# Optimization experiments

Hardware: AMD Instinct MI355X
Metric: run time of the kernel (lower is better)

The kernel has to match this reference:

```python
import jax, jax.numpy as jnp
import numpy as np

N = 50000      # nodes
E = 400000     # edges (before self-loops)
F_IN = 256     # input_dim
HID = 64       # hidden_dim (per-head)
H = 4          # heads
OUT = 16       # output_dim
NEG_SLOPE = 0.2


def _gat_layer(x, W, a_src, a_dst, b, src, dst):
    # x: [N, Fin], W: [Fin, H*HID], a_src/a_dst: [H, HID], b: [H*HID]
    n = x.shape[0]
    h = (x @ W).reshape(n, H, HID)                        # [N,H,D]
    es = jnp.einsum('nhd,hd->nh', h, a_src)               # [N,H]
    ed = jnp.einsum('nhd,hd->nh', h, a_dst)               # [N,H]
    e = jax.nn.leaky_relu(es[src] + ed[dst], NEG_SLOPE)   # [E,H]
    m = jax.ops.segment_max(e, dst, num_segments=n)       # [N,H] segment softmax (stable)
    m = jnp.where(jnp.isfinite(m), m, 0.0)
    p = jnp.exp(e - m[dst])
    s = jax.ops.segment_sum(p, dst, num_segments=n)
    alpha = p / (s[dst] + 1e-16)                          # [E,H]
    out = jax.ops.segment_sum(h[src] * alpha[:, :, None], dst, num_segments=n)  # [N,H,D]
    return out.reshape(n, H * HID) + b


def setup_inputs() -> dict:
    key = jax.random.key(0)
    ks = jax.random.split(key, 24)
    lin = lambda k, i, o: (jax.random.normal(k, (i, o), jnp.float32) / np.sqrt(i)).astype(jnp.float32)
    att = lambda k: (jax.random.normal(k, (H, HID), jnp.float32) * 0.1).astype(jnp.float32)
    FH = H * HID  # 256
    inp = {
        'x': jax.random.normal(ks[0], (N, F_IN), jnp.float32),
        'edge_index': jax.random.randint(ks[1], (2, E), 0, N, dtype=jnp.int64),
        'W1': lin(ks[2], F_IN, FH), 'a1_src': att(ks[3]), 'a1_dst': att(ks[4]), 'b1': jnp.zeros((FH,), jnp.float32),
        'W2': lin(ks[5], FH, FH),   'a2_src': att(ks[6]), 'a2_dst': att(ks[7]), 'b2': jnp.zeros((FH,), jnp.float32),
        'W3': lin(ks[8], FH, FH),   'a3_src': att(ks[9]), 'a3_dst': att(ks[10]), 'b3': jnp.zeros((FH,), jnp.float32),
        'pW1': lin(ks[11], FH, HID), 'pb1': jnp.zeros((HID,), jnp.float32),
        'pW2': lin(ks[12], HID, HID), 'pb2': jnp.zeros((HID,), jnp.float32),
        'cW1': lin(ks[13], FH, HID), 'cb1': jnp.zeros((HID,), jnp.float32),
        'cW2': lin(ks[14], HID, OUT), 'cb2': jnp.zeros((OUT,), jnp.float32),
    }
    return inp


def reference(x, edge_index, W1, a1_src, a1_dst, b1, W2, a2_src, a2_dst, b2,
              W3, a3_src, a3_dst, b3, pW1, pb1, pW2, pb2, cW1, cb1, cW2, cb2):
    n = x.shape[0]
    loop = jnp.arange(n, dtype=edge_index.dtype)          # PyG GATConv adds self-loops
    src = jnp.concatenate([edge_index[0], loop])
    dst = jnp.concatenate([edge_index[1], loop])
    h = jax.nn.elu(_gat_layer(x, W1, a1_src, a1_dst, b1, src, dst))
    h = jax.nn.elu(_gat_layer(h, W2, a2_src, a2_dst, b2, src, dst))
    h = _gat_layer(h, W3, a3_src, a3_dst, b3, src, dst)   # [N, 256]
    logits = jax.nn.relu(h @ cW1 + cb1) @ cW2 + cb2       # classifier (dropout inactive, eval)
    proj = jax.nn.relu(h @ pW1 + pb1) @ pW2 + pb2         # projection head
    return jax.nn.log_softmax(logits, axis=1), proj
```

## Files before the change

kernel.cpp:

```cpp
#include <hip/hip_runtime.h>
#include <hip/hip_bf16.h>

#define NN 50000
#define EE 400000
#define TE (EE + NN)
#define SCAN_B ((NN + 255) / 256)

typedef float f4 __attribute__((ext_vector_type(4)));
typedef __bf16 b8 __attribute__((ext_vector_type(8)));
typedef unsigned short us8 __attribute__((ext_vector_type(8)));

__device__ __forceinline__ float b2f(unsigned short u) {
    union { unsigned int i; float f; } c; c.i = ((unsigned int)u) << 16; return c.f;
}
__device__ __forceinline__ unsigned short f2b(float x) {
    union { unsigned int i; float f; } c; c.f = x;
    unsigned int i = c.i;
    return (unsigned short)((i + 0x7FFFu + ((i >> 16) & 1u)) >> 16);
}
__device__ __forceinline__ int clampi(int v, int lo, int hi) {
    return v < lo ? lo : (v > hi ? hi : v);
}

#define PO_WT    0
#define PO_ATT   196608
#define PO_BT    198912
#define PO_BIAS  231680
#define PO_PW2   231808
#define PO_PB2   235904
#define PO_CW2   235968
#define PO_CB2   236992
#define PO_BT2   237008
#define PO_BIAS2 253392
#define PO_TOTAL 253520

__global__ void detect_kernel(const int* __restrict__ ei, const unsigned int* __restrict__ xw,
                              int* __restrict__ flag) {
    int lane = threadIdx.x;
    int bad = (lane < 16 && ei[2 * lane + 1] != 0) ? 1 : 0;
    int cnt = 0;
#pragma unroll
    for (int k = 0; k < 4; k++) {
        int i = lane + k * 64;
        unsigned short lo = (unsigned short)(xw[i] & 0xFFFFu);
        int e = (lo >> 7) & 0xFF;
        if (e >= 120 && e <= 132) cnt++;
    }
    unsigned long long anybad = __ballot(bad != 0);
#pragma unroll
    for (int off = 1; off < 64; off <<= 1) cnt += __shfl_xor(cnt, off, 64);
    if (lane == 0) {
        flag[0] = (anybad == 0ULL) ? 1 : 0;
        flag[1] = (cnt >= 128) ? 1 : 0;
    }
}

__global__ __launch_bounds__(256) void convx_kernel(const void* __restrict__ src,
                                                    unsigned short* __restrict__ dst,
                                                    const int* __restrict__ flag) {
    int i = blockIdx.x * 256 + threadIdx.x;
    if (i >= NN * 256 / 4) return;
    if (flag[1]) {
        ((ushort4*)dst)[i] = ((const ushort4*)src)[i];
    } else {
        float4 v = ((const float4*)src)[i];
        ushort4 o; o.x = f2b(v.x); o.y = f2b(v.y); o.z = f2b(v.z); o.w = f2b(v.w);
        ((ushort4*)dst)[i] = o;
    }
}

__device__ __forceinline__ float ldf(const void* p, int i, int bf) {
    return bf ? b2f(((const unsigned short*)p)[i]) : ((const float*)p)[i];
}
__global__ __launch_bounds__(256) void prep_kernel(
    const void* W1, const void* W2, const void* W3,
    const void* as1, const void* ad1, const void* b1,
    const void* as2, const void* ad2, const void* b2,
    const void* as3, const void* ad3, const void* b3,
    const void* pW1, const void* pb1, const void* pW2, const void* pb2,
    const void* cW1, const void* cb1, const void* cW2, const void* cb2,
    unsigned short* __restrict__ P, const int* __restrict__ flag) {
    int idx = blockIdx.x * 256 + threadIdx.x;
    if (idx >= PO_TOTAL) return;
    int bf = flag[1];
    float v;
    if (idx < PO_ATT) {
        int l = idx / 65536, r = idx % 65536;
        int n = r >> 8, k = r & 255;
        const void* W = (l == 0) ? W1 : (l == 1) ? W2 : W3;
        v = ldf(W, k * 256 + n, bf);
    } else if (idx < PO_BT) {
        int r = idx - PO_ATT;
        int l = r / 768, w = r % 768, which = w >> 8, j = w & 255;
        const void* s;
        if (which == 0) s = (l == 0) ? as1 : (l == 1) ? as2 : as3;
        else if (which == 1) s = (l == 0) ? ad1 : (l == 1) ? ad2 : ad3;
        else s = (l == 0) ? b1 : (l == 1) ? b2 : b3;
        v = ldf(s, j, bf);
    } else if (idx < PO_BIAS) {
        int r3 = idx - PO_BT;
        int r = r3 >> 8, k = r3 & 255;
        v = (r < 64) ? ldf(cW1, k * 64 + r, bf) : ldf(pW1, k * 64 + (r - 64), bf);
    } else if (idx < PO_PW2) {
        int r = idx - PO_BIAS;
        v = (r < 64) ? ldf(cb1, r, bf) : ldf(pb1, r - 64, bf);
    } else if (idx < PO_PB2) {
        v = ldf(pW2, idx - PO_PW2, bf);
    } else if (idx < PO_CW2) {
        v = ldf(pb2, idx - PO_PB2, bf);
    } else if (idx < PO_CB2) {
        v = ldf(cW2, idx - PO_CW2, bf);
    } else if (idx < PO_BT2) {
        v = ldf(cb2, idx - PO_CB2, bf);
    } else if (idx < PO_BIAS2) {
        int r2 = idx - PO_BT2;
        int r = r2 >> 7, k = r2 & 127;
        if (r < 16) v = (k < 64) ? ldf(cW2, k * 16 + r, bf) : 0.f;
        else if (r < 80) v = (k >= 64) ? ldf(pW2, (k - 64) * 64 + (r - 16), bf) : 0.f;
        else v = 0.f;
    } else {
        int r = idx - PO_BIAS2;
        v = (r < 16) ? ldf(cb2, r, bf) : (r < 80 ? ldf(pb2, r - 16, bf) : 0.f);
    }
    P[idx] = f2b(v);
}

__device__ __forceinline__ void edge_decode(const int* __restrict__ ei, int mode64, int e,
                                            int& src, int& dst) {
    if (e < EE) {
        if (mode64) { src = ei[2 * e]; dst = ei[2 * EE + 2 * e]; }
        else        { src = ei[e];     dst = ei[EE + e]; }
        src = clampi(src, 0, NN - 1);
        dst = clampi(dst, 0, NN - 1);
    } else {
        src = dst = e - EE;
    }
}

__global__ void deg_kernel(const int* __restrict__ ei, const int* __restrict__ flag,
                           int* __restrict__ deg) {
    int e = blockIdx.x * 256 + threadIdx.x;
    if (e >= TE) return;
    int src, dst;
    edge_decode(ei, flag[0], e, src, dst);
    atomicAdd(&deg[dst], 1);
}

__global__ __launch_bounds__(256) void scanA_kernel(const int* __restrict__ deg,
                                                    int* __restrict__ offs, int* __restrict__ bsum) {
    __shared__ int s[256];
    int t = threadIdx.x, i = blockIdx.x * 256 + t;
    int v = (i < NN) ? deg[i] : 0;
    s[t] = v;
    __syncthreads();
    for (int off = 1; off < 256; off <<= 1) {
        int x = (t >= off) ? s[t - off] : 0;
        __syncthreads();
        s[t] += x;
        __syncthreads();
    }
    if (i < NN) offs[i] = s[t] - v;
    if (t == 255) bsum[blockIdx.x] = s[255];
}
__global__ __launch_bounds__(256) void scanB_kernel(int* __restrict__ bsum) {
    __shared__ int s[256];
    int t = threadIdx.x;
    int v = (t < SCAN_B) ? bsum[t] : 0;
    s[t] = v;
    __syncthreads();
    for (int off = 1; off < 256; off <<= 1) {
        int x = (t >= off) ? s[t - off] : 0;
        __syncthreads();
        s[t] += x;
        __syncthreads();
    }
    if (t < SCAN_B) bsum[t] = s[t] - v;
}
__global__ __launch_bounds__(256) void scanC_kernel(int* __restrict__ offs,
                                                    const int* __restrict__ bsum) {
    int t = threadIdx.x, i = blockIdx.x * 256 + t;
    if (i < NN) offs[i] += bsum[blockIdx.x];
    if (i == 0) offs[NN] = TE;
}

__global__ void scatter_kernel(const int* __restrict__ ei, const int* __restrict__ flag,
                               const int* __restrict__ offs,
                               int* __restrict__ cursor, int* __restrict__ srcs) {
    int e = blockIdx.x * 256 + threadIdx.x;
    if (e >= TE) return;
    int src, dst;
    edge_decode(ei, flag[0], e, src, dst);
    int pos = atomicAdd(&cursor[dst], 1);
    int slot = offs[dst] + pos;
    if (slot >= 0 && slot < TE) srcs[slot] = src;
}

__device__ __forceinline__ void async_ld16(const unsigned short* g, unsigned short* l) {
    __builtin_amdgcn_global_load_lds(
        (const __attribute__((address_space(1))) unsigned int*)g,
        (__attribute__((address_space(3))) unsigned int*)l, 16, 0, 0);
}

__global__ __launch_bounds__(256) void gemm_bt_kernel(
    const unsigned short* __restrict__ A, const unsigned short* __restrict__ Bt,
    unsigned short* __restrict__ C, int M, int Nc, int K,
    const unsigned short* __restrict__ bias, int relu, int outf32, int final) {
    __shared__ unsigned short As[128 * 32];
    __shared__ unsigned short Bs[128 * 32];
    int tid = threadIdx.x;
    int lane = tid & 63;
    int wave = tid >> 6;
    int wr = wave >> 1, wc = wave & 1;
    int m0 = blockIdx.x * 128;
    int n0 = blockIdx.y * 128;
    f4 acc[4][4];
#pragma unroll
    for (int i = 0; i < 4; i++)
#pragma unroll
        for (int j = 0; j < 4; j++) acc[i][j] = (f4){0.f, 0.f, 0.f, 0.f};

    int rin = lane >> 2;
    int qsl = lane & 3;
    int qg  = qsl ^ ((rin >> 1) & 3);
    int rsel = lane & 15;
    int q16 = lane >> 4;
    int slotq = q16 ^ ((rsel >> 1) & 3);

    for (int kt = 0; kt < K; kt += 32) {
#pragma unroll
        for (int t = 0; t < 4; t++) {
            int seg = wave * 4 + t;
            if (seg < 8) {
                int r = seg * 16 + rin;
                int gm = m0 + r;
                if (gm < M)
                    async_ld16(A + (size_t)gm * K + kt + qg * 8, &As[seg * 512]);
            } else {
                int r = (seg - 8) * 16 + rin;
                int gn = n0 + r;
                async_ld16(Bt + (size_t)gn * K + kt + qg * 8, &Bs[(seg - 8) * 512]);
            }
        }
        __syncthreads();
        b8 af[4], bfv[4];
#pragma unroll
        for (int i = 0; i < 4; i++) {
            af[i]  = *(const b8*)(&As[(wr * 64 + i * 16 + rsel) * 32 + slotq * 8]);
            bfv[i] = *(const b8*)(&Bs[(wc * 64 + i * 16 + rsel) * 32 + slotq * 8]);
        }
#pragma unroll
        for (int i = 0; i < 4; i++)
#pragma unroll
            for (int j = 0; j < 4; j++)
                acc[i][j] = __builtin_amdgcn_mfma_f32_16x16x32_bf16(af[i], bfv[j], acc[i][j], 0, 0, 0);
        __syncthreads();
    }
    int cl = lane & 15, rq = lane >> 4;
    if (final) {
        float* flog  = (float*)C;
        float* fproj = flog + (size_t)M * 16;
#pragma unroll
        for (int i = 0; i < 4; i++) {
#pragma unroll
            for (int r = 0; r < 4; r++) {
                int row = m0 + wr * 64 + i * 16 + rq * 4 + r;
                if (row >= M) continue;
                if (wc == 0) {
                    float lv = acc[i][0][r] + b2f(bias[cl]);
                    float mx = lv;
#pragma unroll
                    for (int off = 1; off < 16; off <<= 1) mx = fmaxf(mx, __shfl_xor(mx, off, 64));
                    float se = __expf(lv - mx);
#pragma unroll
                    for (int off = 1; off < 16; off <<= 1) se += __shfl_xor(se, off, 64);
                    flog[(size_t)row * 16 + cl] = lv - mx - __logf(se);
#pragma unroll
                    for (int j = 1; j < 4; j++) {
                        float pv = acc[i][j][r] + b2f(bias[j * 16 + cl]);
                        fproj[(size_t)row * 64 + j * 16 + cl - 16] = pv;
                    }
                } else {
                    float pv = acc[i][0][r] + b2f(bias[64 + cl]);
                    fproj[(size_t)row * 64 + 48 + cl] = pv;
                }
            }
        }
        return;
    }
#pragma unroll
    for (int j = 0; j < 4; j++) {
        int col = n0 + wc * 64 + j * 16 + cl;
        float bv = bias ? b2f(bias[col]) : 0.0f;
#pragma unroll
        for (int i = 0; i < 4; i++) {
#pragma unroll
            for (int r = 0; r < 4; r++) {
                int row = m0 + wr * 64 + i * 16 + rq * 4 + r;
                if (row < M) {
                    float v = acc[i][j][r] + bv;
                    if (relu) v = fmaxf(v, 0.0f);
                    if (outf32) ((float*)C)[(size_t)row * Nc + col] = v;
                    else C[(size_t)row * Nc + col] = f2b(v);
                }
            }
        }
    }
}

__global__ __launch_bounds__(256) void esed_kernel(
    const unsigned short* __restrict__ H, const unsigned short* __restrict__ asrc,
    const unsigned short* __restrict__ adst, float* __restrict__ es, float* __restrict__ ed, int N) {
    int gw = (blockIdx.x * 256 + threadIdx.x) >> 6;
    int lane = threadIdx.x & 63;
    if (gw >= N) return;
    int ch = lane << 2;
    int head = lane >> 4;
    int hc = (lane & 15) << 2;
    ushort4 hv = *(const ushort4*)(H + (size_t)gw * 256 + ch);
    ushort4 s4 = *(const ushort4*)(asrc + head * 64 + hc);
    ushort4 d4 = *(const ushort4*)(adst + head * 64 + hc);
    float h0 = b2f(hv.x), h1 = b2f(hv.y), h2 = b2f(hv.z), h3 = b2f(hv.w);
    float s = h0 * b2f(s4.x) + h1 * b2f(s4.y) + h2 * b2f(s4.z) + h3 * b2f(s4.w);
    float d = h0 * b2f(d4.x) + h1 * b2f(d4.y) + h2 * b2f(d4.z) + h3 * b2f(d4.w);
#pragma unroll
    for (int off = 1; off < 16; off <<= 1) {
        s += __shfl_xor(s, off, 64);
        d += __shfl_xor(d, off, 64);
    }
    if ((lane & 15) == 0) { es[gw * 4 + head] = s; ed[gw * 4 + head] = d; }
}

__global__ __launch_bounds__(256) void aggr_kernel(
    const unsigned short* __restrict__ H, const float* __restrict__ es,
    const float* __restrict__ ed,
    const int* __restrict__ offs, const int* __restrict__ srcs,
    const unsigned short* __restrict__ bias, unsigned short* __restrict__ out, int N, int elu) {
    int gw = (blockIdx.x * 256 + threadIdx.x) >> 6;
    int lane = threadIdx.x & 63;
    if (gw >= N) return;
    int half = lane >> 5;
    int lh = lane & 31;
    int ch = lh << 3;
    int head = lh >> 3;
    int j0 = clampi(offs[gw], 0, TE);
    int j1 = clampi(offs[gw + 1], j0, TE);
    float edh = ed[gw * 4 + head];
    float a0 = 0.f, a1 = 0.f, a2 = 0.f, a3 = 0.f;
    float a4 = 0.f, a5 = 0.f, a6 = 0.f, a7 = 0.f;
    float sw = 0.f;
    int j = j0 + half;
    for (; j + 2 < j1; j += 4) {
        int sA = clampi(srcs[j], 0, NN - 1);
        int sB = clampi(srcs[j + 2], 0, NN - 1);
        float qA = es[sA * 4 + head];
        float qB = es[sB * 4 + head];
        us8 hA = *(const us8*)(H + (size_t)sA * 256 + ch);
        us8 hB = *(const us8*)(H + (size_t)sB * 256 + ch);
        float vA = qA + edh; vA = vA > 0.f ? vA : 0.2f * vA;
        float vB = qB + edh; vB = vB > 0.f ? vB : 0.2f * vB;
        float wA = __expf(vA), wB = __expf(vB);
        sw += wA + wB;
        a0 += wA * b2f(hA[0]) + wB * b2f(hB[0]);
        a1 += wA * b2f(hA[1]) + wB * b2f(hB[1]);
        a2 += wA * b2f(hA[2]) + wB * b2f(hB[2]);
        a3 += wA * b2f(hA[3]) + wB * b2f(hB[3]);
        a4 += wA * b2f(hA[4]) + wB * b2f(hB[4]);
        a5 += wA * b2f(hA[5]) + wB * b2f(hB[5]);
        a6 += wA * b2f(hA[6]) + wB * b2f(hB[6]);
        a7 += wA * b2f(hA[7]) + wB * b2f(hB[7]);
    }
    for (; j < j1; j += 2) {
        int sA = clampi(srcs[j], 0, NN - 1);
        float qA = es[sA * 4 + head];
        us8 hA = *(const us8*)(H + (size_t)sA * 256 + ch);
        float vA = qA + edh; vA = vA > 0.f ? vA : 0.2f * vA;
        float wA = __expf(vA);
        sw += wA;
        a0 += wA * b2f(hA[0]); a1 += wA * b2f(hA[1]);
        a2 += wA * b2f(hA[2]); a3 += wA * b2f(hA[3]);
        a4 += wA * b2f(hA[4]); a5 += wA * b2f(hA[5]);
        a6 += wA * b2f(hA[6]); a7 += wA * b2f(hA[7]);
    }
    sw += __shfl_xor(sw, 32, 64);
    a0 += __shfl_xor(a0, 32, 64); a1 += __shfl_xor(a1, 32, 64);
    a2 += __shfl_xor(a2, 32, 64); a3 += __shfl_xor(a3, 32, 64);
    a4 += __shfl_xor(a4, 32, 64); a5 += __shfl_xor(a5, 32, 64);
    a6 += __shfl_xor(a6, 32, 64); a7 += __shfl_xor(a7, 32, 64);
    if (half == 0) {
        float rs = 1.f / (sw + 1e-16f);
        us8 bv = *(const us8*)(bias + ch);
        float r0 = a0 * rs + b2f(bv[0]), r1 = a1 * rs + b2f(bv[1]);
        float r2 = a2 * rs + b2f(bv[2]), r3 = a3 * rs + b2f(bv[3]);
        float r4 = a4 * rs + b2f(bv[4]), r5 = a5 * rs + b2f(bv[5]);
        float r6 = a6 * rs + b2f(bv[6]), r7 = a7 * rs + b2f(bv[7]);
        if (elu) {
            r0 = r0 > 0.f ? r0 : __expf(r0) - 1.f;
            r1 = r1 > 0.f ? r1 : __expf(r1) - 1.f;
            r2 = r2 > 0.f ? r2 : __expf(r2) - 1.f;
            r3 = r3 > 0.f ? r3 : __expf(r3) - 1.f;
            r4 = r4 > 0.f ? r4 : __expf(r4) - 1.f;
            r5 = r5 > 0.f ? r5 : __expf(r5) - 1.f;
            r6 = r6 > 0.f ? r6 : __expf(r6) - 1.f;
            r7 = r7 > 0.f ? r7 : __expf(r7) - 1.f;
        }
        us8 o;
        o[0] = f2b(r0); o[1] = f2b(r1); o[2] = f2b(r2); o[3] = f2b(r3);
        o[4] = f2b(r4); o[5] = f2b(r5); o[6] = f2b(r6); o[7] = f2b(r7);
        *(us8*)(out + (size_t)gw * 256 + ch) = o;
    }
}

extern "C" void kernel_launch(void* const* d_in, const int* in_sizes, int n_in,
                              void* d_out, int out_size, void* d_ws, size_t ws_size,
                              hipStream_t stream) {
    (void)in_sizes; (void)n_in; (void)out_size; (void)ws_size;
    const int* ei = (const int*)d_in[1];

    char* p = (char*)d_ws;
    auto take = [&](size_t bytes) -> void* {
        void* r = (void*)p;
        p += (bytes + 255) & ~(size_t)255;
        return r;
    };
    int* flag   = (int*)take(256);
    int* deg    = (int*)take((size_t)NN * 4);
    int* cursor = (int*)take((size_t)NN * 4);
    int* offs   = (int*)take((size_t)(NN + 1) * 4);
    int* bsum   = (int*)take(256 * 4);
    int* srcs   = (int*)take((size_t)TE * 4);
    float* es   = (float*)take((size_t)NN * 16);
    float* ed   = (float*)take((size_t)NN * 16);
    unsigned short* bufH = (unsigned short*)take((size_t)NN * 256 * 2);
    unsigned short* buf1 = (unsigned short*)take((size_t)NN * 256 * 2);
    unsigned short* buf2 = (unsigned short*)take((size_t)NN * 256 * 2);
    unsigned short* P    = (unsigned short*)take((size_t)PO_TOTAL * 2);
    unsigned short* xb = buf2;
    unsigned short* tbuf = bufH;

    detect_kernel<<<1, 64, 0, stream>>>(ei, (const unsigned int*)d_in[0], flag);
    convx_kernel<<<NN * 256 / 4 / 256, 256, 0, stream>>>(d_in[0], xb, flag);
    prep_kernel<<<(PO_TOTAL + 255) / 256, 256, 0, stream>>>(
        d_in[2], d_in[6], d_in[10],
        d_in[3], d_in[4], d_in[5],
        d_in[7], d_in[8], d_in[9],
        d_in[11], d_in[12], d_in[13],
        d_in[14], d_in[15], d_in[16], d_in[17],
        d_in[18], d_in[19], d_in[20], d_in[21],
        P, flag);

    hipMemsetAsync(deg, 0, (size_t)NN * 4, stream);
    hipMemsetAsync(cursor, 0, (size_t)NN * 4, stream);
    deg_kernel<<<(TE + 255) / 256, 256, 0, stream>>>(ei, flag, deg);
    scanA_kernel<<<SCAN_B, 256, 0, stream>>>(deg, offs, bsum);
    scanB_kernel<<<1, 256, 0, stream>>>(bsum);
    scanC_kernel<<<SCAN_B, 256, 0, stream>>>(offs, bsum);
    scatter_kernel<<<(TE + 255) / 256, 256, 0, stream>>>(ei, flag, offs, cursor, srcs);

    const unsigned short* X = xb;
    unsigned short* outbuf[3] = {buf1, buf2, buf1};
    for (int l = 0; l < 3; l++) {
        const unsigned short* Wt  = P + PO_WT + l * 65536;
        const unsigned short* asr = P + PO_ATT + l * 768;
        const unsigned short* adr = P + PO_ATT + l * 768 + 256;
        const unsigned short* bcb = P + PO_ATT + l * 768 + 512;
        gemm_bt_kernel<<<dim3((NN + 127) / 128, 2), 256, 0, stream>>>(X, Wt, bufH, NN, 256, 256, nullptr, 0, 0, 0);
        esed_kernel<<<12500, 256, 0, stream>>>(bufH, asr, adr, es, ed, NN);
        aggr_kernel<<<12500, 256, 0, stream>>>(bufH, es, ed, offs, srcs, bcb, outbuf[l], NN, (l < 2) ? 1 : 0);
        X = outbuf[l];
    }
    gemm_bt_kernel<<<dim3((NN + 127) / 128, 1), 256, 0, stream>>>(X, P + PO_BT, tbuf, NN, 128, 256, P + PO_BIAS, 1, 0, 0);
    gemm_bt_kernel<<<dim3((NN + 127) / 128, 1), 256, 0, stream>>>(tbuf, P + PO_BT2, (unsigned short*)d_out, NN, 128, 128, P + PO_BIAS2, 0, 0, 1);
}
```

Measured before the change: 442.9 us.

## Fuse attention scores into GEMM epilogue and precompute per-edge exp weights

```diff
diff --git a/kernel.cpp b/kernel.cpp
--- a/kernel.cpp
+++ b/kernel.cpp
@@ -185,14 +185,15 @@
 
 __global__ void scatter_kernel(const int* __restrict__ ei, const int* __restrict__ flag,
                                const int* __restrict__ offs,
-                               int* __restrict__ cursor, int* __restrict__ srcs) {
+                               int* __restrict__ cursor, int* __restrict__ srcs,
+                               int* __restrict__ dsts) {
     int e = blockIdx.x * 256 + threadIdx.x;
     if (e >= TE) return;
     int src, dst;
     edge_decode(ei, flag[0], e, src, dst);
     int pos = atomicAdd(&cursor[dst], 1);
     int slot = offs[dst] + pos;
-    if (slot >= 0 && slot < TE) srcs[slot] = src;
+    if (slot >= 0 && slot < TE) { srcs[slot] = src; dsts[slot] = dst; }
 }
 
 __device__ __forceinline__ void async_ld16(const unsigned short* g, unsigned short* l) {
@@ -204,7 +205,9 @@
 __global__ __launch_bounds__(256) void gemm_bt_kernel(
     const unsigned short* __restrict__ A, const unsigned short* __restrict__ Bt,
     unsigned short* __restrict__ C, int M, int Nc, int K,
-    const unsigned short* __restrict__ bias, int relu, int outf32, int final) {
+    const unsigned short* __restrict__ bias, int relu, int outf32, int final,
+    const unsigned short* __restrict__ asrc, const unsigned short* __restrict__ adst,
+    float* __restrict__ es, float* __restrict__ ed) {
     __shared__ unsigned short As[128 * 32];
     __shared__ unsigned short Bs[128 * 32];
     int tid = threadIdx.x;
@@ -256,6 +259,47 @@
         __syncthreads();
     }
     int cl = lane & 15, rq = lane >> 4;
+    if (es) {
+        int head = blockIdx.y * 2 + wc;
+        float asv[4], adv[4];
+#pragma unroll
+        for (int j = 0; j < 4; j++) {
+            asv[j] = b2f(asrc[head * 64 + j * 16 + cl]);
+            adv[j] = b2f(adst[head * 64 + j * 16 + cl]);
+        }
+#pragma unroll
+        for (int i = 0; i < 4; i++) {
+            float pes[4], ped[4];
+#pragma unroll
+            for (int r = 0; r < 4; r++) {
+                float se = 0.f, de = 0.f;
+#pragma unroll
+                for (int j = 0; j < 4; j++) {
+                    se += acc[i][j][r] * asv[j];
+                    de += acc[i][j][r] * adv[j];
+                }
+                pes[r] = se; ped[r] = de;
+            }
+#pragma unroll
+            for (int off = 1; off < 16; off <<= 1) {
+#pragma unroll
+                for (int r = 0; r < 4; r++) {
+                    pes[r] += __shfl_xor(pes[r], off, 64);
+                    ped[r] += __shfl_xor(ped[r], off, 64);
+                }
+            }
+            if (cl == 0) {
+#pragma unroll
+                for (int r = 0; r < 4; r++) {
+                    int row = m0 + wr * 64 + i * 16 + rq * 4 + r;
+                    if (row < M) {
+                        es[(size_t)row * 4 + head] = pes[r];
+                        ed[(size_t)row * 4 + head] = ped[r];
+                    }
+                }
+            }
+        }
+    }
     if (final) {
         float* flog  = (float*)C;
         float* fproj = flog + (size_t)M * 16;
@@ -307,32 +351,23 @@
     }
 }
 
-__global__ __launch_bounds__(256) void esed_kernel(
-    const unsigned short* __restrict__ H, const unsigned short* __restrict__ asrc,
-    const unsigned short* __restrict__ adst, float* __restrict__ es, float* __restrict__ ed, int N) {
-    int gw = (blockIdx.x * 256 + threadIdx.x) >> 6;
-    int lane = threadIdx.x & 63;
-    if (gw >= N) return;
-    int ch = lane << 2;
-    int head = lane >> 4;
-    int hc = (lane & 15) << 2;
-    ushort4 hv = *(const ushort4*)(H + (size_t)gw * 256 + ch);
-    ushort4 s4 = *(const ushort4*)(asrc + head * 64 + hc);
-    ushort4 d4 = *(const ushort4*)(adst + head * 64 + hc);
-    float h0 = b2f(hv.x), h1 = b2f(hv.y), h2 = b2f(hv.z), h3 = b2f(hv.w);
-    float s = h0 * b2f(s4.x) + h1 * b2f(s4.y) + h2 * b2f(s4.z) + h3 * b2f(s4.w);
-    float d = h0 * b2f(d4.x) + h1 * b2f(d4.y) + h2 * b2f(d4.z) + h3 * b2f(d4.w);
-#pragma unroll
-    for (int off = 1; off < 16; off <<= 1) {
-        s += __shfl_xor(s, off, 64);
-        d += __shfl_xor(d, off, 64);
-    }
-    if ((lane & 15) == 0) { es[gw * 4 + head] = s; ed[gw * 4 + head] = d; }
+__global__ __launch_bounds__(256) void wexp_kernel(
+    const float* __restrict__ es, const float* __restrict__ ed,
+    const int* __restrict__ srcs, const int* __restrict__ dsts,
+    float* __restrict__ wbuf) {
+    int j = blockIdx.x * 256 + threadIdx.x;
+    if (j >= TE) return;
+    int s = srcs[j], d = dsts[j];
+    float4 a = ((const float4*)es)[s];
+    float4 b = ((const float4*)ed)[d];
+    float v0 = a.x + b.x, v1 = a.y + b.y, v2 = a.z + b.z, v3 = a.w + b.w;
+    v0 = v0 > 0.f ? v0 : 0.2f * v0; v1 = v1 > 0.f ? v1 : 0.2f * v1;
+    v2 = v2 > 0.f ? v2 : 0.2f * v2; v3 = v3 > 0.f ? v3 : 0.2f * v3;
+    ((float4*)wbuf)[j] = make_float4(__expf(v0), __expf(v1), __expf(v2), __expf(v3));
 }
 
 __global__ __launch_bounds__(256) void aggr_kernel(
-    const unsigned short* __restrict__ H, const float* __restrict__ es,
-    const float* __restrict__ ed,
+    const unsigned short* __restrict__ H, const float* __restrict__ wbuf,
     const int* __restrict__ offs, const int* __restrict__ srcs,
     const unsigned short* __restrict__ bias, unsigned short* __restrict__ out, int N, int elu) {
     int gw = (blockIdx.x * 256 + threadIdx.x) >> 6;
@@ -342,23 +377,20 @@
     int lh = lane & 31;
     int ch = lh << 3;
     int head = lh >> 3;
-    int j0 = clampi(offs[gw], 0, TE);
-    int j1 = clampi(offs[gw + 1], j0, TE);
-    float edh = ed[gw * 4 + head];
+    int j0 = offs[gw];
+    int j1 = offs[gw + 1];
     float a0 = 0.f, a1 = 0.f, a2 = 0.f, a3 = 0.f;
     float a4 = 0.f, a5 = 0.f, a6 = 0.f, a7 = 0.f;
     float sw = 0.f;
-    int j = j0 + half;
-    for (; j + 2 < j1; j += 4) {
-        int sA = clampi(srcs[j], 0, NN - 1);
-        int sB = clampi(srcs[j + 2], 0, NN - 1);
-        float qA = es[sA * 4 + head];
-        float qB = es[sB * 4 + head];
+    int nfull = (j1 - j0) & ~3;
+    int jb = j0 + half * 2;
+    for (int t = 0; t < nfull; t += 4) {
+        int sA = srcs[jb + t];
+        int sB = srcs[jb + t + 1];
+        float wA = wbuf[(size_t)(jb + t) * 4 + head];
+        float wB = wbuf[(size_t)(jb + t + 1) * 4 + head];
         us8 hA = *(const us8*)(H + (size_t)sA * 256 + ch);
         us8 hB = *(const us8*)(H + (size_t)sB * 256 + ch);
-        float vA = qA + edh; vA = vA > 0.f ? vA : 0.2f * vA;
-        float vB = qB + edh; vB = vB > 0.f ? vB : 0.2f * vB;
-        float wA = __expf(vA), wB = __expf(vB);
         sw += wA + wB;
         a0 += wA * b2f(hA[0]) + wB * b2f(hB[0]);
         a1 += wA * b2f(hA[1]) + wB * b2f(hB[1]);
@@ -369,12 +401,10 @@
         a6 += wA * b2f(hA[6]) + wB * b2f(hB[6]);
         a7 += wA * b2f(hA[7]) + wB * b2f(hB[7]);
     }
-    for (; j < j1; j += 2) {
-        int sA = clampi(srcs[j], 0, NN - 1);
-        float qA = es[sA * 4 + head];
+    for (int j = j0 + nfull + half; j < j1; j += 2) {
+        int sA = srcs[j];
+        float wA = wbuf[(size_t)j * 4 + head];
         us8 hA = *(const us8*)(H + (size_t)sA * 256 + ch);
-        float vA = qA + edh; vA = vA > 0.f ? vA : 0.2f * vA;
-        float wA = __expf(vA);
         sw += wA;
         a0 += wA * b2f(hA[0]); a1 += wA * b2f(hA[1]);
         a2 += wA * b2f(hA[2]); a3 += wA * b2f(hA[3]);
@@ -428,8 +458,10 @@
     int* offs   = (int*)take((size_t)(NN + 1) * 4);
     int* bsum   = (int*)take(256 * 4);
     int* srcs   = (int*)take((size_t)TE * 4);
+    int* dsts   = (int*)take((size_t)TE * 4);
     float* es   = (float*)take((size_t)NN * 16);
     float* ed   = (float*)take((size_t)NN * 16);
+    float* wbuf = (float*)take((size_t)TE * 16);
     unsigned short* bufH = (unsigned short*)take((size_t)NN * 256 * 2);
     unsigned short* buf1 = (unsigned short*)take((size_t)NN * 256 * 2);
     unsigned short* buf2 = (unsigned short*)take((size_t)NN * 256 * 2);
@@ -454,7 +486,7 @@
     scanA_kernel<<<SCAN_B, 256, 0, stream>>>(deg, offs, bsum);
     scanB_kernel<<<1, 256, 0, stream>>>(bsum);
     scanC_kernel<<<SCAN_B, 256, 0, stream>>>(offs, bsum);
-    scatter_kernel<<<(TE + 255) / 256, 256, 0, stream>>>(ei, flag, offs, cursor, srcs);
+    scatter_kernel<<<(TE + 255) / 256, 256, 0, stream>>>(ei, flag, offs, cursor, srcs, dsts);
 
     const unsigned short* X = xb;
     unsigned short* outbuf[3] = {buf1, buf2, buf1};
@@ -463,11 +495,14 @@
         const unsigned short* asr = P + PO_ATT + l * 768;
         const unsigned short* adr = P + PO_ATT + l * 768 + 256;
         const unsigned short* bcb = P + PO_ATT + l * 768 + 512;
-        gemm_bt_kernel<<<dim3((NN + 127) / 128, 2), 256, 0, stream>>>(X, Wt, bufH, NN, 256, 256, nullptr, 0, 0, 0);
-        esed_kernel<<<12500, 256, 0, stream>>>(bufH, asr, adr, es, ed, NN);
-        aggr_kernel<<<12500, 256, 0, stream>>>(bufH, es, ed, offs, srcs, bcb, outbuf[l], NN, (l < 2) ? 1 : 0);
+        gemm_bt_kernel<<<dim3((NN + 127) / 128, 2), 256, 0, stream>>>(
+            X, Wt, bufH, NN, 256, 256, nullptr, 0, 0, 0, asr, adr, es, ed);
+        wexp_kernel<<<(TE + 255) / 256, 256, 0, stream>>>(es, ed, srcs, dsts, wbuf);
+        aggr_kernel<<<12500, 256, 0, stream>>>(bufH, wbuf, offs, srcs, bcb, outbuf[l], NN, (l < 2) ? 1 : 0);
         X = outbuf[l];
     }
-    gemm_bt_kernel<<<dim3((NN + 127) / 128, 1), 256, 0, stream>>>(X, P + PO_BT, tbuf, NN, 128, 256, P + PO_BIAS, 1, 0, 0);
-    gemm_bt_kernel<<<dim3((NN + 127) / 128, 1), 256, 0, stream>>>(tbuf, P + PO_BT2, (unsigned short*)d_out, NN, 128, 128, P + PO_BIAS2, 0, 0, 1);
-}
+    gemm_bt_kernel<<<dim3((NN + 127) / 128, 1), 256, 0, stream>>>(
+        X, P + PO_BT, tbuf, NN, 128, 256, P + PO_BIAS, 1, 0, 0, nullptr, nullptr, nullptr, nullptr);
+    gemm_bt_kernel<<<dim3((NN + 127) / 128, 1), 256, 0, stream>>>(
+        tbuf, P + PO_BT2, (unsigned short*)d_out, NN, 128, 128, P + PO_BIAS2, 0, 0, 1, nullptr, nullptr, nullptr, nullptr);
+}
```

Measured after the change: 442.6 us. About the same (-0.1%).
